# Kernel tuning notes

Hardware: AMD Instinct MI355X
Metric: run time of the kernel (lower is better)

The kernel has to match this reference:

```python
import jax, jax.numpy as jnp
import numpy as np

NEG_SLOPE = 0.2  # LeakyReLU slope from the module


def setup_inputs() -> dict:
    key = jax.random.key(0)
    k1, k2, k3, k4 = jax.random.split(key, 4)
    B, N, C, H, D = 8, 1024, 256, 4, 64
    x = jax.random.normal(k1, (B, N, C), dtype=jnp.float32)
    adj = (jax.random.uniform(k2, (B, N, N)) < 0.05).astype(jnp.float32)
    # nn.Linear weight, stored as (in, out) for x @ W
    W = jax.random.normal(k3, (C, H * D), dtype=jnp.float32) / np.sqrt(C)
    a = jax.random.normal(k4, (1, H, 2 * D), dtype=jnp.float32) * 0.1
    return {"x": x, "adj": adj, "W": W, "a": a}


def reference(x, adj, W, a):
    # x: (B,N,C), adj: (B,N,N), W: (C,H*D), a: (1,H,2D)
    B, N, _ = x.shape
    H = a.shape[1]
    D = a.shape[2] // 2
    Wx = (x @ W).reshape(B, N, H, D)  # (B,N,H,D)
    # (cat([Wx_i, Wx_j]) * a).sum(-1) decomposes into two rank-1 terms:
    a_i, a_j = a[0, :, :D], a[0, :, D:]
    e_i = jnp.einsum('bnhd,hd->bnh', Wx, a_i)  # contribution of target node i
    e_j = jnp.einsum('bjhd,hd->bjh', Wx, a_j)  # contribution of source node j
    e = e_i[:, :, None, :] + e_j[:, None, :, :]  # (B,N,N,H)
    e = jnp.where(e > 0, e, NEG_SLOPE * e)  # LeakyReLU(0.2)
    # add self-loops, mask non-edges with -inf
    adj_self = adj + jnp.eye(N, dtype=adj.dtype)[None]
    mask = (adj_self == 0)[..., None]  # (B,N,N,1)
    e = jnp.where(mask, -jnp.inf, e)
    alpha = jax.nn.softmax(e, axis=2)  # softmax over neighbors j
    # dropout is identity in eval mode
    # torch: einsum('bnjh,bnjhd', alpha, Wx_j) with Wx_j broadcast over n
    out = jnp.einsum('bnjh,bjhd->bnhd', alpha, Wx)
    return out.reshape(B, N, H * D)
```

## Files before the change

kernel.cpp:

```cpp
#include <hip/hip_runtime.h>

#define Nn 1024
#define Cc 256
#define Hh 4
#define Dd 64
#define HD 256
#define LOG2E 1.4426950408889634f

typedef unsigned short u16;
typedef unsigned int u32;
typedef unsigned long long u64;
typedef unsigned char u8;
typedef __bf16 bf16x8 __attribute__((ext_vector_type(8)));
typedef float f32x4 __attribute__((ext_vector_type(4)));
typedef u16 u16x8 __attribute__((ext_vector_type(8)));

__device__ __forceinline__ float bf2f(u16 v) {
    return __builtin_bit_cast(float, (u32)v << 16);
}
__device__ __forceinline__ u16 f2bf(float f) {
    u32 u = __builtin_bit_cast(u32, f);
    return (u16)((u + 0x7fffu + ((u >> 16) & 1u)) >> 16);
}
__device__ __forceinline__ float leaky(float s) {
    return fmaxf(s, 0.2f * s);
}

__global__ void k_prep_w(const float* __restrict__ W, u16* __restrict__ WTh,
                         u16* __restrict__ WTl) {
    int c = blockIdx.x;
    int t = threadIdx.x;
    float v = W[c * HD + t];
    u16 hi = f2bf(v);
    float lo = v - bf2f(hi);
    WTh[t * Cc + c] = hi;
    WTl[t * Cc + c] = f2bf(lo);
}

__global__ __launch_bounds__(256) void k_gemm_xw(const float* __restrict__ x,
        const u16* __restrict__ WTh, const u16* __restrict__ WTl,
        const float* __restrict__ a, u16* __restrict__ WxTt,
        float* __restrict__ ei, float* __restrict__ ej) {
    int wave = blockIdx.x * 4 + (threadIdx.x >> 6);
    int lane = threadIdx.x & 63;
    int row_tile = wave >> 2;
    int h = wave & 3;
    int m0 = row_tile * 16;
    int b = m0 >> 10;
    int nloc0 = m0 & 1023;
    int c15 = lane & 15;
    int quad = lane >> 4;

    f32x4 acc[4] = {};
    const float* xrow = x + (size_t)(m0 + c15) * Cc + quad * 8;
    #pragma unroll
    for (int k0 = 0; k0 < Cc; k0 += 32) {
        float4 xv0 = *reinterpret_cast<const float4*>(xrow + k0);
        float4 xv1 = *reinterpret_cast<const float4*>(xrow + k0 + 4);
        float xv[8] = {xv0.x, xv0.y, xv0.z, xv0.w, xv1.x, xv1.y, xv1.z, xv1.w};
        u16x8 xh, xl;
        #pragma unroll
        for (int i = 0; i < 8; ++i) {
            u16 hb = f2bf(xv[i]);
            xh[i] = hb;
            xl[i] = f2bf(xv[i] - bf2f(hb));
        }
        bf16x8 ah = __builtin_bit_cast(bf16x8, xh);
        bf16x8 al = __builtin_bit_cast(bf16x8, xl);
        #pragma unroll
        for (int t = 0; t < 4; ++t) {
            const u16* wb = WTh + (size_t)(h * 64 + t * 16 + c15) * Cc + k0 + quad * 8;
            const u16* wl = WTl + (size_t)(h * 64 + t * 16 + c15) * Cc + k0 + quad * 8;
            bf16x8 bh = *reinterpret_cast<const bf16x8*>(wb);
            bf16x8 bl = *reinterpret_cast<const bf16x8*>(wl);
            acc[t] = __builtin_amdgcn_mfma_f32_16x16x32_bf16(ah, bh, acc[t], 0, 0, 0);
            acc[t] = __builtin_amdgcn_mfma_f32_16x16x32_bf16(al, bh, acc[t], 0, 0, 0);
            acc[t] = __builtin_amdgcn_mfma_f32_16x16x32_bf16(ah, bl, acc[t], 0, 0, 0);
        }
    }
    int bh = b * Hh + h;
    int n_base = nloc0 + quad * 4;
    int chunk = nloc0 >> 5;
    int jq = ((n_base >> 3) & 3);
    int ii = n_base & 7;
    size_t tb = (size_t)bh * 65536 + chunk * 2048 + jq * 128 + c15 * 8 + ii;
    #pragma unroll
    for (int t = 0; t < 4; ++t) {
        u32 lo = (u32)f2bf(acc[t][0]) | ((u32)f2bf(acc[t][1]) << 16);
        u32 hi = (u32)f2bf(acc[t][2]) | ((u32)f2bf(acc[t][3]) << 16);
        uint2 pk; pk.x = lo; pk.y = hi;
        *reinterpret_cast<uint2*>(WxTt + tb + t * 512) = pk;
    }
    float ai[4], aj[4];
    #pragma unroll
    for (int t = 0; t < 4; ++t) {
        ai[t] = a[h * 2 * Dd + t * 16 + c15];
        aj[t] = a[h * 2 * Dd + Dd + t * 16 + c15];
    }
    #pragma unroll
    for (int r = 0; r < 4; ++r) {
        float si = acc[0][r] * ai[0] + acc[1][r] * ai[1] + acc[2][r] * ai[2] + acc[3][r] * ai[3];
        float sj = acc[0][r] * aj[0] + acc[1][r] * aj[1] + acc[2][r] * aj[2] + acc[3][r] * aj[3];
        #pragma unroll
        for (int off = 1; off < 16; off <<= 1) {
            si += __shfl_xor(si, off);
            sj += __shfl_xor(sj, off);
        }
        if (c15 == 0) {
            int n = nloc0 + quad * 4 + r;
            ei[(size_t)bh * Nn + n] = si;
            ej[(size_t)bh * Nn + n] = sj;
        }
    }
}

__global__ __launch_bounds__(256) void k_bitmask(const float* __restrict__ adj,
                                                 u8* __restrict__ bm) {
    int idx = blockIdx.x * 256 + threadIdx.x;
    int bn = idx >> 7;
    int byteidx = idx & 127;
    int n = bn & 1023;
    const float* p = adj + ((size_t)bn << 10) + (byteidx << 3);
    float4 v0 = *reinterpret_cast<const float4*>(p);
    float4 v1 = *reinterpret_cast<const float4*>(p + 4);
    u32 bits = 0;
    bits |= (__builtin_bit_cast(u32, v0.x) != 0u) ? 1u : 0u;
    bits |= (__builtin_bit_cast(u32, v0.y) != 0u) ? 2u : 0u;
    bits |= (__builtin_bit_cast(u32, v0.z) != 0u) ? 4u : 0u;
    bits |= (__builtin_bit_cast(u32, v0.w) != 0u) ? 8u : 0u;
    bits |= (__builtin_bit_cast(u32, v1.x) != 0u) ? 16u : 0u;
    bits |= (__builtin_bit_cast(u32, v1.y) != 0u) ? 32u : 0u;
    bits |= (__builtin_bit_cast(u32, v1.z) != 0u) ? 64u : 0u;
    bits |= (__builtin_bit_cast(u32, v1.w) != 0u) ? 128u : 0u;
    if ((n >> 3) == byteidx) bits |= 1u << (n & 7);
    bm[idx] = (u8)bits;
}

__global__ __launch_bounds__(256) void k_attn(const u8* __restrict__ bm,
        const u16* __restrict__ WxTt, const float* __restrict__ ei,
        const float* __restrict__ ejp, float* __restrict__ out) {
    int wave = blockIdx.x * 4 + (threadIdx.x >> 6);
    int lane = threadIdx.x & 63;
    int bh = wave >> 6;
    int ntile = wave & 63;
    int b = bh >> 2, h = bh & 3;
    int n0 = ntile * 16;
    int col = lane & 15;
    int quad = lane >> 4;

    int nrow = n0 + col;
    float ei_r = ei[(size_t)bh * Nn + nrow];

    const u8* mbrow = bm + ((size_t)(b * Nn + nrow)) * 128;
    const float* ejrow = ejp + (size_t)bh * Nn + quad * 8;
    const u16* wxplane = WxTt + (size_t)bh * 65536 + lane * 8;

    f32x4 acc[4] = {};
    float lsum = 0.f;
    for (int j0 = 0; j0 < Nn; j0 += 32) {
        u32 mb32 = *reinterpret_cast<const u32*>(mbrow + (j0 >> 3));
        u32 mbits = (mb32 >> (quad * 8)) & 0xffu;
        float4 ej0 = *reinterpret_cast<const float4*>(ejrow + j0);
        float4 ej1 = *reinterpret_cast<const float4*>(ejrow + j0 + 4);
        float ejv[8] = {ej0.x, ej0.y, ej0.z, ej0.w, ej1.x, ej1.y, ej1.z, ej1.w};
        u16x8 au;
        #pragma unroll
        for (int i = 0; i < 8; ++i) {
            float s = leaky(ei_r + ejv[i]);
            float p = exp2f(s * LOG2E);
            p = ((mbits >> i) & 1u) ? p : 0.f;
            lsum += p;
            au[i] = f2bf(p);
        }
        bf16x8 afr = __builtin_bit_cast(bf16x8, au);
        const u16* bbase = wxplane + (j0 >> 5) * 2048;
        #pragma unroll
        for (int t = 0; t < 4; ++t) {
            bf16x8 bfr = *reinterpret_cast<const bf16x8*>(bbase + t * 512);
            acc[t] = __builtin_amdgcn_mfma_f32_16x16x32_bf16(afr, bfr, acc[t], 0, 0, 0);
        }
    }
    lsum += __shfl_xor(lsum, 16);
    lsum += __shfl_xor(lsum, 32);
    #pragma unroll
    for (int r = 0; r < 4; ++r) {
        int rloc = quad * 4 + r;
        float lv = __shfl(lsum, rloc);
        float inv = 1.0f / lv;
        int nr = n0 + rloc;
        size_t obase = ((size_t)(b * Nn + nr)) * HD + h * Dd;
        #pragma unroll
        for (int t = 0; t < 4; ++t) {
            out[obase + t * 16 + col] = acc[t][r] * inv;
        }
    }
}

extern "C" void kernel_launch(void* const* d_in, const int* in_sizes, int n_in,
                              void* d_out, int out_size, void* d_ws, size_t ws_size,
                              hipStream_t stream) {
    const float* x   = (const float*)d_in[0];
    const float* adj = (const float*)d_in[1];
    const float* W   = (const float*)d_in[2];
    const float* a   = (const float*)d_in[3];
    float* out = (float*)d_out;

    char* ws = (char*)d_ws;
    u16*   WTh  = (u16*)(ws);
    u16*   WTl  = (u16*)(ws + (128u << 10));
    u16*   WxTt = (u16*)(ws + (256u << 10));
    float* ei   = (float*)(ws + (256u << 10) + (4u << 20));
    float* ej   = (float*)(ws + (384u << 10) + (4u << 20));
    u8*    bm   = (u8*)(ws + (512u << 10) + (4u << 20));

    k_prep_w<<<256, 256, 0, stream>>>(W, WTh, WTl);
    k_gemm_xw<<<512, 256, 0, stream>>>(x, WTh, WTl, a, WxTt, ei, ej);
    k_bitmask<<<4096, 256, 0, stream>>>(adj, bm);
    k_attn<<<512, 256, 0, stream>>>(bm, WxTt, ei, ej, out);
}
```

Baseline: 127.6 us.

## Split attention over neighbor chunks per wave, fuse W prep into bitmask kernel

```diff
diff --git a/kernel.cpp b/kernel.cpp
--- a/kernel.cpp
+++ b/kernel.cpp
@@ -14,6 +14,7 @@
 typedef __bf16 bf16x8 __attribute__((ext_vector_type(8)));
 typedef float f32x4 __attribute__((ext_vector_type(4)));
 typedef u16 u16x8 __attribute__((ext_vector_type(8)));
+typedef u32 u32x4 __attribute__((ext_vector_type(4)));
 
 __device__ __forceinline__ float bf2f(u16 v) {
     return __builtin_bit_cast(float, (u32)v << 16);
@@ -22,100 +23,17 @@
     u32 u = __builtin_bit_cast(u32, f);
     return (u16)((u + 0x7fffu + ((u >> 16) & 1u)) >> 16);
 }
-__device__ __forceinline__ float leaky(float s) {
-    return fmaxf(s, 0.2f * s);
-}
-
-__global__ void k_prep_w(const float* __restrict__ W, u16* __restrict__ WTh,
-                         u16* __restrict__ WTl) {
-    int c = blockIdx.x;
-    int t = threadIdx.x;
-    float v = W[c * HD + t];
-    u16 hi = f2bf(v);
-    float lo = v - bf2f(hi);
-    WTh[t * Cc + c] = hi;
-    WTl[t * Cc + c] = f2bf(lo);
-}
-
-__global__ __launch_bounds__(256) void k_gemm_xw(const float* __restrict__ x,
-        const u16* __restrict__ WTh, const u16* __restrict__ WTl,
-        const float* __restrict__ a, u16* __restrict__ WxTt,
-        float* __restrict__ ei, float* __restrict__ ej) {
-    int wave = blockIdx.x * 4 + (threadIdx.x >> 6);
-    int lane = threadIdx.x & 63;
-    int row_tile = wave >> 2;
-    int h = wave & 3;
-    int m0 = row_tile * 16;
-    int b = m0 >> 10;
-    int nloc0 = m0 & 1023;
-    int c15 = lane & 15;
-    int quad = lane >> 4;
-
-    f32x4 acc[4] = {};
-    const float* xrow = x + (size_t)(m0 + c15) * Cc + quad * 8;
-    #pragma unroll
-    for (int k0 = 0; k0 < Cc; k0 += 32) {
-        float4 xv0 = *reinterpret_cast<const float4*>(xrow + k0);
-        float4 xv1 = *reinterpret_cast<const float4*>(xrow + k0 + 4);
-        float xv[8] = {xv0.x, xv0.y, xv0.z, xv0.w, xv1.x, xv1.y, xv1.z, xv1.w};
-        u16x8 xh, xl;
-        #pragma unroll
-        for (int i = 0; i < 8; ++i) {
-            u16 hb = f2bf(xv[i]);
-            xh[i] = hb;
-            xl[i] = f2bf(xv[i] - bf2f(hb));
-        }
-        bf16x8 ah = __builtin_bit_cast(bf16x8, xh);
-        bf16x8 al = __builtin_bit_cast(bf16x8, xl);
-        #pragma unroll
-        for (int t = 0; t < 4; ++t) {
-            const u16* wb = WTh + (size_t)(h * 64 + t * 16 + c15) * Cc + k0 + quad * 8;
-            const u16* wl = WTl + (size_t)(h * 64 + t * 16 + c15) * Cc + k0 + quad * 8;
-            bf16x8 bh = *reinterpret_cast<const bf16x8*>(wb);
-            bf16x8 bl = *reinterpret_cast<const bf16x8*>(wl);
-            acc[t] = __builtin_amdgcn_mfma_f32_16x16x32_bf16(ah, bh, acc[t], 0, 0, 0);
-            acc[t] = __builtin_amdgcn_mfma_f32_16x16x32_bf16(al, bh, acc[t], 0, 0, 0);
-            acc[t] = __builtin_amdgcn_mfma_f32_16x16x32_bf16(ah, bl, acc[t], 0, 0, 0);
-        }
-    }
-    int bh = b * Hh + h;
-    int n_base = nloc0 + quad * 4;
-    int chunk = nloc0 >> 5;
-    int jq = ((n_base >> 3) & 3);
-    int ii = n_base & 7;
-    size_t tb = (size_t)bh * 65536 + chunk * 2048 + jq * 128 + c15 * 8 + ii;
-    #pragma unroll
-    for (int t = 0; t < 4; ++t) {
-        u32 lo = (u32)f2bf(acc[t][0]) | ((u32)f2bf(acc[t][1]) << 16);
-        u32 hi = (u32)f2bf(acc[t][2]) | ((u32)f2bf(acc[t][3]) << 16);
-        uint2 pk; pk.x = lo; pk.y = hi;
-        *reinterpret_cast<uint2*>(WxTt + tb + t * 512) = pk;
-    }
-    float ai[4], aj[4];
-    #pragma unroll
-    for (int t = 0; t < 4; ++t) {
-        ai[t] = a[h * 2 * Dd + t * 16 + c15];
-        aj[t] = a[h * 2 * Dd + Dd + t * 16 + c15];
-    }
-    #pragma unroll
-    for (int r = 0; r < 4; ++r) {
-        float si = acc[0][r] * ai[0] + acc[1][r] * ai[1] + acc[2][r] * ai[2] + acc[3][r] * ai[3];
-        float sj = acc[0][r] * aj[0] + acc[1][r] * aj[1] + acc[2][r] * aj[2] + acc[3][r] * aj[3];
-        #pragma unroll
-        for (int off = 1; off < 16; off <<= 1) {
-            si += __shfl_xor(si, off);
-            sj += __shfl_xor(sj, off);
-        }
-        if (c15 == 0) {
-            int n = nloc0 + quad * 4 + r;
-            ei[(size_t)bh * Nn + n] = si;
-            ej[(size_t)bh * Nn + n] = sj;
-        }
-    }
-}
-
-__global__ __launch_bounds__(256) void k_bitmask(const float* __restrict__ adj,
-                                                 u8* __restrict__ bm) {
+__device__ __forceinline__ float fast_exp2(float x) {
+#if __has_builtin(__builtin_amdgcn_exp2f)
+    return __builtin_amdgcn_exp2f(x);
+#else
+    float r; asm("v_exp_f32 %0, %1" : "=v"(r) : "v"(x)); return r;
+#endif
+}
+
+__global__ __launch_bounds__(256) void k_bitmask_prep(const float* __restrict__ adj,
+        u8* __restrict__ bm, const float* __restrict__ W,
+        u16* __restrict__ WTh, u16* __restrict__ WTl) {
     int idx = blockIdx.x * 256 + threadIdx.x;
     int bn = idx >> 7;
     int byteidx = idx & 127;
@@ -134,64 +52,195 @@
     bits |= (__builtin_bit_cast(u32, v1.w) != 0u) ? 128u : 0u;
     if ((n >> 3) == byteidx) bits |= 1u << (n & 7);
     bm[idx] = (u8)bits;
-}
-
-__global__ __launch_bounds__(256) void k_attn(const u8* __restrict__ bm,
-        const u16* __restrict__ WxTt, const float* __restrict__ ei,
-        const float* __restrict__ ejp, float* __restrict__ out) {
+    if (blockIdx.x < 256) {
+        int c = blockIdx.x;
+        int t = threadIdx.x;
+        float v = W[c * HD + t];
+        u16 hi = f2bf(v);
+        float lo = v - bf2f(hi);
+        WTh[t * Cc + c] = hi;
+        WTl[t * Cc + c] = f2bf(lo);
+    }
+}
+
+__global__ __launch_bounds__(256) void k_gemm_xw(const float* __restrict__ x,
+        const u16* __restrict__ WTh, const u16* __restrict__ WTl,
+        const float* __restrict__ a, u16* __restrict__ WxTt,
+        float* __restrict__ ei, float* __restrict__ ej) {
     int wave = blockIdx.x * 4 + (threadIdx.x >> 6);
     int lane = threadIdx.x & 63;
-    int bh = wave >> 6;
-    int ntile = wave & 63;
+    int row_tile = wave >> 2;
+    int h = wave & 3;
+    int m0 = row_tile * 16;
+    int b = m0 >> 10;
+    int nloc0 = m0 & 1023;
+    int c15 = lane & 15;
+    int quad = lane >> 4;
+
+    f32x4 acc[4] = {};
+    const float* xrow = x + (size_t)(m0 + c15) * Cc + quad * 8;
+    #pragma unroll
+    for (int k0 = 0; k0 < Cc; k0 += 32) {
+        float4 xv0 = *reinterpret_cast<const float4*>(xrow + k0);
+        float4 xv1 = *reinterpret_cast<const float4*>(xrow + k0 + 4);
+        float xv[8] = {xv0.x, xv0.y, xv0.z, xv0.w, xv1.x, xv1.y, xv1.z, xv1.w};
+        u16x8 xh, xl;
+        #pragma unroll
+        for (int i = 0; i < 8; ++i) {
+            u16 hb = f2bf(xv[i]);
+            xh[i] = hb;
+            xl[i] = f2bf(xv[i] - bf2f(hb));
+        }
+        bf16x8 ah = __builtin_bit_cast(bf16x8, xh);
+        bf16x8 al = __builtin_bit_cast(bf16x8, xl);
+        #pragma unroll
+        for (int t = 0; t < 4; ++t) {
+            const u16* wb = WTh + (size_t)(h * 64 + t * 16 + c15) * Cc + k0 + quad * 8;
+            const u16* wl = WTl + (size_t)(h * 64 + t * 16 + c15) * Cc + k0 + quad * 8;
+            bf16x8 bh = *reinterpret_cast<const bf16x8*>(wb);
+            bf16x8 bl = *reinterpret_cast<const bf16x8*>(wl);
+            acc[t] = __builtin_amdgcn_mfma_f32_16x16x32_bf16(ah, bh, acc[t], 0, 0, 0);
+            acc[t] = __builtin_amdgcn_mfma_f32_16x16x32_bf16(al, bh, acc[t], 0, 0, 0);
+            acc[t] = __builtin_amdgcn_mfma_f32_16x16x32_bf16(ah, bl, acc[t], 0, 0, 0);
+        }
+    }
+    int bh = b * Hh + h;
+    int n_base = nloc0 + quad * 4;
+    int chunk = nloc0 >> 5;
+    int jq = ((n_base >> 3) & 3);
+    int ii = n_base & 7;
+    size_t tb = (size_t)bh * 65536 + chunk * 2048 + jq * 128 + c15 * 8 + ii;
+    #pragma unroll
+    for (int t = 0; t < 4; ++t) {
+        u32 lo = (u32)f2bf(acc[t][0]) | ((u32)f2bf(acc[t][1]) << 16);
+        u32 hi = (u32)f2bf(acc[t][2]) | ((u32)f2bf(acc[t][3]) << 16);
+        uint2 pk; pk.x = lo; pk.y = hi;
+        *reinterpret_cast<uint2*>(WxTt + tb + t * 512) = pk;
+    }
+    float ai[4], aj[4];
+    #pragma unroll
+    for (int t = 0; t < 4; ++t) {
+        ai[t] = a[h * 2 * Dd + t * 16 + c15];
+        aj[t] = a[h * 2 * Dd + Dd + t * 16 + c15];
+    }
+    #pragma unroll
+    for (int r = 0; r < 4; ++r) {
+        float si = acc[0][r] * ai[0] + acc[1][r] * ai[1] + acc[2][r] * ai[2] + acc[3][r] * ai[3];
+        float sj = acc[0][r] * aj[0] + acc[1][r] * aj[1] + acc[2][r] * aj[2] + acc[3][r] * aj[3];
+        #pragma unroll
+        for (int off = 1; off < 16; off <<= 1) {
+            si += __shfl_xor(si, off);
+            sj += __shfl_xor(sj, off);
+        }
+        if (c15 == 0) {
+            int n = nloc0 + quad * 4 + r;
+            ei[(size_t)bh * Nn + n] = si * LOG2E;
+            ej[(size_t)bh * Nn + n] = sj * LOG2E;
+        }
+    }
+}
+
+__global__ __launch_bounds__(256) void k_attn(const u8* __restrict__ bm,
+        const u16* __restrict__ WxTt, const float* __restrict__ eis,
+        const float* __restrict__ ejs, float* __restrict__ out) {
+    int widx = threadIdx.x >> 6;
+    int lane = threadIdx.x & 63;
+    int bh = blockIdx.x >> 5;
+    int tile = blockIdx.x & 31;
     int b = bh >> 2, h = bh & 3;
-    int n0 = ntile * 16;
+    int n0 = tile * 32;
     int col = lane & 15;
     int quad = lane >> 4;
 
-    int nrow = n0 + col;
-    float ei_r = ei[(size_t)bh * Nn + nrow];
-
-    const u8* mbrow = bm + ((size_t)(b * Nn + nrow)) * 128;
-    const float* ejrow = ejp + (size_t)bh * Nn + quad * 8;
+    int r0 = n0 + col, r1 = n0 + 16 + col;
+    float ei0 = eis[(size_t)bh * Nn + r0];
+    float ei1 = eis[(size_t)bh * Nn + r1];
+    const u8* mb0 = bm + ((size_t)(b * Nn + r0)) * 128;
+    const u8* mb1 = bm + ((size_t)(b * Nn + r1)) * 128;
+    const float* ejrow = ejs + (size_t)bh * Nn + quad * 8;
     const u16* wxplane = WxTt + (size_t)bh * 65536 + lane * 8;
 
-    f32x4 acc[4] = {};
-    float lsum = 0.f;
-    for (int j0 = 0; j0 < Nn; j0 += 32) {
-        u32 mb32 = *reinterpret_cast<const u32*>(mbrow + (j0 >> 3));
-        u32 mbits = (mb32 >> (quad * 8)) & 0xffu;
-        float4 ej0 = *reinterpret_cast<const float4*>(ejrow + j0);
-        float4 ej1 = *reinterpret_cast<const float4*>(ejrow + j0 + 4);
-        float ejv[8] = {ej0.x, ej0.y, ej0.z, ej0.w, ej1.x, ej1.y, ej1.z, ej1.w};
-        u16x8 au;
-        #pragma unroll
-        for (int i = 0; i < 8; ++i) {
-            float s = leaky(ei_r + ejv[i]);
-            float p = exp2f(s * LOG2E);
-            p = ((mbits >> i) & 1u) ? p : 0.f;
-            lsum += p;
-            au[i] = f2bf(p);
-        }
-        bf16x8 afr = __builtin_bit_cast(bf16x8, au);
+    u16 ov = (col == 0) ? (u16)0x3f80 : (u16)0;
+    u16x8 onesu = {ov, ov, ov, ov, ov, ov, ov, ov};
+    bf16x8 onesf = __builtin_bit_cast(bf16x8, onesu);
+
+    f32x4 acc0[4] = {}, acc1[4] = {};
+    f32x4 accl0 = {}, accl1 = {};
+    int jbase = widx * 256;
+    #pragma unroll 2
+    for (int s = 0; s < 8; ++s) {
+        int j0 = jbase + s * 32;
+        u32 mw0 = *reinterpret_cast<const u32*>(mb0 + (j0 >> 3));
+        u32 mw1 = *reinterpret_cast<const u32*>(mb1 + (j0 >> 3));
+        u32 q0 = (mw0 >> (quad * 8)) & 0xffu;
+        u32 q1 = (mw1 >> (quad * 8)) & 0xffu;
+        float4 eA = *reinterpret_cast<const float4*>(ejrow + j0);
+        float4 eB = *reinterpret_cast<const float4*>(ejrow + j0 + 4);
+        float ejv[8] = {eA.x, eA.y, eA.z, eA.w, eB.x, eB.y, eB.z, eB.w};
+        u32 p0[4], p1[4];
+        #pragma unroll
+        for (int pi = 0; pi < 4; ++pi) {
+            float e_lo = ejv[2 * pi], e_hi = ejv[2 * pi + 1];
+            float sa = ei0 + e_lo, sb = ei0 + e_hi;
+            sa = fmaxf(sa, 0.2f * sa); sb = fmaxf(sb, 0.2f * sb);
+            u32 ua = __builtin_bit_cast(u32, fast_exp2(sa));
+            u32 ub = __builtin_bit_cast(u32, fast_exp2(sb));
+            u32 m0 = (((q0 >> (2 * pi)) & 1u) ? 0xffffu : 0u)
+                   | (((q0 >> (2 * pi + 1)) & 1u) ? 0xffff0000u : 0u);
+            p0[pi] = ((ua >> 16) | (ub & 0xffff0000u)) & m0;
+            float sc = ei1 + e_lo, sd = ei1 + e_hi;
+            sc = fmaxf(sc, 0.2f * sc); sd = fmaxf(sd, 0.2f * sd);
+            u32 uc = __builtin_bit_cast(u32, fast_exp2(sc));
+            u32 ud = __builtin_bit_cast(u32, fast_exp2(sd));
+            u32 m1 = (((q1 >> (2 * pi)) & 1u) ? 0xffffu : 0u)
+                   | (((q1 >> (2 * pi + 1)) & 1u) ? 0xffff0000u : 0u);
+            p1[pi] = ((uc >> 16) | (ud & 0xffff0000u)) & m1;
+        }
+        u32x4 pv0 = {p0[0], p0[1], p0[2], p0[3]};
+        u32x4 pv1 = {p1[0], p1[1], p1[2], p1[3]};
+        bf16x8 a0 = __builtin_bit_cast(bf16x8, pv0);
+        bf16x8 a1 = __builtin_bit_cast(bf16x8, pv1);
         const u16* bbase = wxplane + (j0 >> 5) * 2048;
         #pragma unroll
         for (int t = 0; t < 4; ++t) {
             bf16x8 bfr = *reinterpret_cast<const bf16x8*>(bbase + t * 512);
-            acc[t] = __builtin_amdgcn_mfma_f32_16x16x32_bf16(afr, bfr, acc[t], 0, 0, 0);
-        }
-    }
-    lsum += __shfl_xor(lsum, 16);
-    lsum += __shfl_xor(lsum, 32);
-    #pragma unroll
-    for (int r = 0; r < 4; ++r) {
-        int rloc = quad * 4 + r;
-        float lv = __shfl(lsum, rloc);
-        float inv = 1.0f / lv;
-        int nr = n0 + rloc;
-        size_t obase = ((size_t)(b * Nn + nr)) * HD + h * Dd;
-        #pragma unroll
-        for (int t = 0; t < 4; ++t) {
-            out[obase + t * 16 + col] = acc[t][r] * inv;
+            acc0[t] = __builtin_amdgcn_mfma_f32_16x16x32_bf16(a0, bfr, acc0[t], 0, 0, 0);
+            acc1[t] = __builtin_amdgcn_mfma_f32_16x16x32_bf16(a1, bfr, acc1[t], 0, 0, 0);
+        }
+        accl0 = __builtin_amdgcn_mfma_f32_16x16x32_bf16(a0, onesf, accl0, 0, 0, 0);
+        accl1 = __builtin_amdgcn_mfma_f32_16x16x32_bf16(a1, onesf, accl1, 0, 0, 0);
+    }
+
+    __shared__ f32x4 lacc[4][8][64];
+    __shared__ float lsums[4][2][16];
+    #pragma unroll
+    for (int t = 0; t < 4; ++t) {
+        lacc[widx][t][lane] = acc0[t];
+        lacc[widx][4 + t][lane] = acc1[t];
+    }
+    if (col == 0) {
+        #pragma unroll
+        for (int r = 0; r < 4; ++r) {
+            lsums[widx][0][quad * 4 + r] = accl0[r];
+            lsums[widx][1][quad * 4 + r] = accl1[r];
+        }
+    }
+    __syncthreads();
+    #pragma unroll
+    for (int pp = 0; pp < 2; ++pp) {
+        int p = widx * 2 + pp;
+        int f = p >> 2, t = p & 3;
+        f32x4 v = lacc[0][p][lane];
+        v += lacc[1][p][lane];
+        v += lacc[2][p][lane];
+        v += lacc[3][p][lane];
+        #pragma unroll
+        for (int r = 0; r < 4; ++r) {
+            int rloc = quad * 4 + r;
+            float lv = lsums[0][f][rloc] + lsums[1][f][rloc]
+                     + lsums[2][f][rloc] + lsums[3][f][rloc];
+            int nr = n0 + f * 16 + rloc;
+            out[(size_t)(b * Nn + nr) * HD + h * Dd + t * 16 + col] = v[r] * (1.0f / lv);
         }
     }
 }
@@ -213,8 +262,7 @@
     float* ej   = (float*)(ws + (384u << 10) + (4u << 20));
     u8*    bm   = (u8*)(ws + (512u << 10) + (4u << 20));
 
-    k_prep_w<<<256, 256, 0, stream>>>(W, WTh, WTl);
+    k_bitmask_prep<<<4096, 256, 0, stream>>>(adj, bm, W, WTh, WTl);
     k_gemm_xw<<<512, 256, 0, stream>>>(x, WTh, WTl, a, WxTt, ei, ej);
-    k_bitmask<<<4096, 256, 0, stream>>>(adj, bm);
-    k_attn<<<512, 256, 0, stream>>>(bm, WxTt, ei, ej, out);
-}
+    k_attn<<<1024, 256, 0, stream>>>(bm, WxTt, ei, ej, out);
+}
```

Result: faster. 124.9 us (-2.1%).
